# Kernel optimization log

Measured on AMD Instinct MI355X. Metric: run time of the kernel, lower is better.

## Reference

```python
import jax, jax.numpy as jnp
import numpy as np

B, S, D_IN, D_OUT = 4, 2048, 4096, 4096
ACT_CLIP = 6.0

def setup_inputs() -> dict:
    key = jax.random.key(0)
    k1, k2, k3, k4 = jax.random.split(key, 4)
    x = jax.random.normal(k1, (B, S, D_IN), dtype=jnp.float32)
    # symmetric int8 weights in [-127, 127] (stored as int8)
    weight_i8 = jax.random.randint(k2, (D_OUT, D_IN), -127, 128, dtype=jnp.int32).astype(jnp.int8)
    # per-output-channel positive scales, ~ max|w|/127 magnitude
    weight_scale = (jax.random.uniform(k3, (D_OUT,), dtype=jnp.float32) * 0.02 + 1e-4)
    bias = jax.random.normal(k4, (D_OUT,), dtype=jnp.float32)
    return {"x": x, "weight_i8": weight_i8, "weight_scale": weight_scale, "bias": bias}

def reference(x, weight_i8, weight_scale, bias):
    # activation clip
    x = jnp.clip(x, -ACT_CLIP, ACT_CLIP)
    # per-channel dequant: weight[o, i] = i8[o, i] * scale[o]
    weight = weight_i8.astype(jnp.float32) * weight_scale[:, None]
    weight = weight.astype(x.dtype)
    # F.linear: x @ weight.T + bias
    out = jnp.einsum('bsi,oi->bso', x, weight) + bias.astype(x.dtype)
    return out
```

## Files before the change

### kernel.cpp

```cpp
#include <hip/hip_runtime.h>
#include <stdint.h>
#include <stddef.h>


#define M_DIM 8192
#define N_DIM 4096
#define K_DIM 4096
#define ACT_CLIP 6.0f

#define BM 256
#define BN 256
#define BKI 64
#define NKT (K_DIM / BKI)
#define TILE_LDS 32768
#define RING 4

typedef __attribute__((ext_vector_type(4))) int i32x4;
typedef __attribute__((ext_vector_type(16))) int i32x16;

__device__ __forceinline__ void async_load16(const void* g, void* l) {
    __builtin_amdgcn_global_load_lds(
        (const __attribute__((address_space(1))) void*)g,
        (__attribute__((address_space(3))) void*)l, 16, 0, 0);
}

__global__ __launch_bounds__(256) void quant_x_kernel(
    const float* __restrict__ x, int8_t* __restrict__ xq,
    float* __restrict__ rowscale) {
    const int row = blockIdx.x;
    const int tid = threadIdx.x;
    const float4* xr = (const float4*)(x + (size_t)row * K_DIM);
    float4 v[4];
    float mx = 0.f;
#pragma unroll
    for (int c = 0; c < 4; ++c) {
        float4 a = xr[c * 256 + tid];
        a.x = fminf(ACT_CLIP, fmaxf(-ACT_CLIP, a.x));
        a.y = fminf(ACT_CLIP, fmaxf(-ACT_CLIP, a.y));
        a.z = fminf(ACT_CLIP, fmaxf(-ACT_CLIP, a.z));
        a.w = fminf(ACT_CLIP, fmaxf(-ACT_CLIP, a.w));
        v[c] = a;
        mx = fmaxf(mx, fmaxf(fmaxf(fabsf(a.x), fabsf(a.y)),
                             fmaxf(fabsf(a.z), fabsf(a.w))));
    }
#pragma unroll
    for (int off = 32; off >= 1; off >>= 1)
        mx = fmaxf(mx, __shfl_xor(mx, off, 64));
    __shared__ float wmax[4];
    if ((tid & 63) == 0) wmax[tid >> 6] = mx;
    __syncthreads();
    mx = fmaxf(fmaxf(wmax[0], wmax[1]), fmaxf(wmax[2], wmax[3]));
    mx = fmaxf(mx, 1e-20f);
    const float inv = 127.f / mx;
    if (tid == 0) rowscale[row] = mx * (1.f / 127.f);
    int* out = (int*)(xq + (size_t)row * K_DIM);
#pragma unroll
    for (int c = 0; c < 4; ++c) {
        int b0 = (int)rintf(v[c].x * inv);
        int b1 = (int)rintf(v[c].y * inv);
        int b2 = (int)rintf(v[c].z * inv);
        int b3 = (int)rintf(v[c].w * inv);
        out[c * 256 + tid] =
            (b0 & 255) | ((b1 & 255) << 8) | ((b2 & 255) << 16) | ((b3 & 255) << 24);
    }
}

__global__ __launch_bounds__(256) void pack_w_kernel(
    const int* __restrict__ w, int8_t* __restrict__ wq) {
    size_t idx = (size_t)blockIdx.x * blockDim.x + threadIdx.x;
    const int4* w4 = (const int4*)w;
    int r[4];
#pragma unroll
    for (int j = 0; j < 4; ++j) {
        int4 a = w4[idx * 4 + j];
        r[j] = (a.x & 255) | ((a.y & 255) << 8) | ((a.z & 255) << 16) | ((a.w & 255) << 24);
    }
    ((int4*)wq)[idx] = make_int4(r[0], r[1], r[2], r[3]);
}

__global__ __launch_bounds__(512, 2) void gemm_i8_kernel(
    const int8_t* __restrict__ A, const int8_t* __restrict__ Bw,
    const float* __restrict__ rowscale, const float* __restrict__ scale,
    const float* __restrict__ bias, float* __restrict__ out) {
    extern __shared__ __align__(16) int8_t smem[];

    const int tid = threadIdx.x;
    const int wave = tid >> 6;
    const int lane = tid & 63;
    const int l31 = lane & 31;
    const int hi = lane >> 5;
    const int m0 = blockIdx.y * BM;
    const int n0 = blockIdx.x * BN;
    const int wm = (wave >> 2) * 128;
    const int wn = (wave & 3) * 64;

    const int8_t* ga[2];
    const int8_t* gb[2];
    int lbA[2], lbB[2];
#pragma unroll
    for (int j = 0; j < 2; ++j) {
        const int s = tid + 512 * j;
        const int row = s >> 2;
        const int c = (s & 3) ^ ((row >> 1) & 3);
        ga[j] = A + (size_t)(m0 + row) * K_DIM + c * 16;
        gb[j] = Bw + (size_t)(n0 + row) * K_DIM + c * 16;
        lbA[j] = (wave * 64 + 512 * j) * 16;
        lbB[j] = 16384 + (wave * 64 + 512 * j) * 16;
    }

    auto STAGE = [&](int b) {
        int8_t* buf = smem + b * TILE_LDS;
#pragma unroll
        for (int j = 0; j < 2; ++j) async_load16(ga[j], buf + lbA[j]);
#pragma unroll
        for (int j = 0; j < 2; ++j) async_load16(gb[j], buf + lbB[j]);
#pragma unroll
        for (int j = 0; j < 2; ++j) { ga[j] += BKI; gb[j] += BKI; }
    };

    int aoff[4][2], boff[2][2];
#pragma unroll
    for (int mt = 0; mt < 4; ++mt)
#pragma unroll
        for (int ks = 0; ks < 2; ++ks) {
            const int row = wm + mt * 32 + l31;
            const int c = ks * 2 + hi;
            aoff[mt][ks] = (row * 4 + (c ^ ((row >> 1) & 3))) * 16;
        }
#pragma unroll
    for (int nt = 0; nt < 2; ++nt)
#pragma unroll
        for (int ks = 0; ks < 2; ++ks) {
            const int row = wn + nt * 32 + l31;
            const int c = ks * 2 + hi;
            boff[nt][ks] = 16384 + (row * 4 + (c ^ ((row >> 1) & 3))) * 16;
        }

    i32x16 acc[4][2] = {};

    STAGE(0);
    STAGE(1);

    for (int t = 0; t < NKT; ++t) {
        if (t + 2 < NKT) STAGE((t + 2) & 3);
        if (t < NKT - 2) {
            asm volatile("s_waitcnt vmcnt(8)" ::: "memory");
        } else if (t == NKT - 2) {
            asm volatile("s_waitcnt vmcnt(4)" ::: "memory");
        } else {
            asm volatile("s_waitcnt vmcnt(0)" ::: "memory");
        }
        asm volatile("s_barrier" ::: "memory");

        const int8_t* buf = smem + (t & 3) * TILE_LDS;
#pragma unroll
        for (int ks = 0; ks < 2; ++ks) {
            i32x4 af[4], bf[2];
#pragma unroll
            for (int mt = 0; mt < 4; ++mt)
                af[mt] = *(const i32x4*)(buf + aoff[mt][ks]);
#pragma unroll
            for (int nt = 0; nt < 2; ++nt)
                bf[nt] = *(const i32x4*)(buf + boff[nt][ks]);
            __builtin_amdgcn_s_setprio(1);
#pragma unroll
            for (int mt = 0; mt < 4; ++mt)
#pragma unroll
                for (int nt = 0; nt < 2; ++nt)
                    acc[mt][nt] = __builtin_amdgcn_mfma_i32_32x32x32_i8(
                        af[mt], bf[nt], acc[mt][nt], 0, 0, 0);
            __builtin_amdgcn_s_setprio(0);
        }
    }

    const int ccol = l31;
#pragma unroll
    for (int mt = 0; mt < 4; ++mt) {
        const int gmb = m0 + wm + mt * 32;
        float rs[16];
#pragma unroll
        for (int r = 0; r < 16; ++r)
            rs[r] = rowscale[gmb + (r & 3) + 4 * hi + 8 * (r >> 2)];
#pragma unroll
        for (int nt = 0; nt < 2; ++nt) {
            const int gn = n0 + wn + nt * 32 + ccol;
            const float sc = scale[gn];
            const float bi = bias[gn];
            float* op = out + (size_t)gmb * N_DIM + gn;
#pragma unroll
            for (int r = 0; r < 16; ++r) {
                const int grow = (r & 3) + 4 * hi + 8 * (r >> 2);
                op[(size_t)grow * N_DIM] =
                    fmaf((float)acc[mt][nt][r], rs[r] * sc, bi);
            }
        }
    }
}

extern "C" void kernel_launch(void* const* d_in, const int* in_sizes, int n_in,
                              void* d_out, int out_size, void* d_ws, size_t ws_size,
                              hipStream_t stream) {
    const float* x = (const float*)d_in[0];
    const int* w_i8 = (const int*)d_in[1];
    const float* w_scale = (const float*)d_in[2];
    const float* bias = (const float*)d_in[3];
    float* out = (float*)d_out;

    int8_t* xq = (int8_t*)d_ws;
    int8_t* wq = (int8_t*)d_ws + (size_t)M_DIM * K_DIM;
    float* rowscale = (float*)((int8_t*)d_ws + (size_t)M_DIM * K_DIM
                               + (size_t)N_DIM * K_DIM);

    static bool attr_done = false;
    if (!attr_done) {
        hipFuncSetAttribute((const void*)gemm_i8_kernel,
                            hipFuncAttributeMaxDynamicSharedMemorySize,
                            RING * TILE_LDS);
        attr_done = true;
    }

    quant_x_kernel<<<M_DIM, 256, 0, stream>>>(x, xq, rowscale);
    pack_w_kernel<<<(size_t)N_DIM * K_DIM / (16 * 256), 256, 0, stream>>>(w_i8, wq);

    dim3 grid(N_DIM / BN, M_DIM / BM);
    gemm_i8_kernel<<<grid, 512, RING * TILE_LDS, stream>>>(
        xq, wq, rowscale, w_scale, bias, out);
}
```

Baseline: 404.3 us.

## Software-pipeline LDS reads with MFMA in int8 GEMM and merge prep kernels

Restructures the GEMM main loop so LDS fragment reads for the next k-substep are issued before the MFMAs of the current one, with a three-stage prefetch depth and one barrier per tile. It also merges the activation-quantize and weight-pack kernels into a single launch with a branch on block index. The goals are to hide LDS latency behind matrix math and to remove one kernel launch and its tail. It costs more fragment registers under the 2-waves-per-SIMD launch bound, which risks spills.

```diff
diff --git a/kernel.cpp b/kernel.cpp
--- a/kernel.cpp
+++ b/kernel.cpp
@@ -24,58 +24,59 @@
         (__attribute__((address_space(3))) void*)l, 16, 0, 0);
 }
 
-__global__ __launch_bounds__(256) void quant_x_kernel(
+__global__ __launch_bounds__(256) void prep_kernel(
     const float* __restrict__ x, int8_t* __restrict__ xq,
-    float* __restrict__ rowscale) {
-    const int row = blockIdx.x;
+    float* __restrict__ rowscale,
+    const int* __restrict__ w, int8_t* __restrict__ wq) {
     const int tid = threadIdx.x;
-    const float4* xr = (const float4*)(x + (size_t)row * K_DIM);
-    float4 v[4];
-    float mx = 0.f;
-#pragma unroll
-    for (int c = 0; c < 4; ++c) {
-        float4 a = xr[c * 256 + tid];
-        a.x = fminf(ACT_CLIP, fmaxf(-ACT_CLIP, a.x));
-        a.y = fminf(ACT_CLIP, fmaxf(-ACT_CLIP, a.y));
-        a.z = fminf(ACT_CLIP, fmaxf(-ACT_CLIP, a.z));
-        a.w = fminf(ACT_CLIP, fmaxf(-ACT_CLIP, a.w));
-        v[c] = a;
-        mx = fmaxf(mx, fmaxf(fmaxf(fabsf(a.x), fabsf(a.y)),
-                             fmaxf(fabsf(a.z), fabsf(a.w))));
-    }
-#pragma unroll
-    for (int off = 32; off >= 1; off >>= 1)
-        mx = fmaxf(mx, __shfl_xor(mx, off, 64));
-    __shared__ float wmax[4];
-    if ((tid & 63) == 0) wmax[tid >> 6] = mx;
-    __syncthreads();
-    mx = fmaxf(fmaxf(wmax[0], wmax[1]), fmaxf(wmax[2], wmax[3]));
-    mx = fmaxf(mx, 1e-20f);
-    const float inv = 127.f / mx;
-    if (tid == 0) rowscale[row] = mx * (1.f / 127.f);
-    int* out = (int*)(xq + (size_t)row * K_DIM);
-#pragma unroll
-    for (int c = 0; c < 4; ++c) {
-        int b0 = (int)rintf(v[c].x * inv);
-        int b1 = (int)rintf(v[c].y * inv);
-        int b2 = (int)rintf(v[c].z * inv);
-        int b3 = (int)rintf(v[c].w * inv);
-        out[c * 256 + tid] =
-            (b0 & 255) | ((b1 & 255) << 8) | ((b2 & 255) << 16) | ((b3 & 255) << 24);
-    }
-}
-
-__global__ __launch_bounds__(256) void pack_w_kernel(
-    const int* __restrict__ w, int8_t* __restrict__ wq) {
-    size_t idx = (size_t)blockIdx.x * blockDim.x + threadIdx.x;
-    const int4* w4 = (const int4*)w;
-    int r[4];
-#pragma unroll
-    for (int j = 0; j < 4; ++j) {
-        int4 a = w4[idx * 4 + j];
-        r[j] = (a.x & 255) | ((a.y & 255) << 8) | ((a.z & 255) << 16) | ((a.w & 255) << 24);
-    }
-    ((int4*)wq)[idx] = make_int4(r[0], r[1], r[2], r[3]);
+    if (blockIdx.x < M_DIM) {
+        const int row = blockIdx.x;
+        const float4* xr = (const float4*)(x + (size_t)row * K_DIM);
+        float4 v[4];
+        float mx = 0.f;
+#pragma unroll
+        for (int c = 0; c < 4; ++c) {
+            float4 a = xr[c * 256 + tid];
+            a.x = fminf(ACT_CLIP, fmaxf(-ACT_CLIP, a.x));
+            a.y = fminf(ACT_CLIP, fmaxf(-ACT_CLIP, a.y));
+            a.z = fminf(ACT_CLIP, fmaxf(-ACT_CLIP, a.z));
+            a.w = fminf(ACT_CLIP, fmaxf(-ACT_CLIP, a.w));
+            v[c] = a;
+            mx = fmaxf(mx, fmaxf(fmaxf(fabsf(a.x), fabsf(a.y)),
+                                 fmaxf(fabsf(a.z), fabsf(a.w))));
+        }
+#pragma unroll
+        for (int off = 32; off >= 1; off >>= 1)
+            mx = fmaxf(mx, __shfl_xor(mx, off, 64));
+        __shared__ float wmax[4];
+        if ((tid & 63) == 0) wmax[tid >> 6] = mx;
+        __syncthreads();
+        mx = fmaxf(fmaxf(wmax[0], wmax[1]), fmaxf(wmax[2], wmax[3]));
+        mx = fmaxf(mx, 1e-20f);
+        const float inv = 127.f / mx;
+        if (tid == 0) rowscale[row] = mx * (1.f / 127.f);
+        int* out = (int*)(xq + (size_t)row * K_DIM);
+#pragma unroll
+        for (int c = 0; c < 4; ++c) {
+            int b0 = (int)rintf(v[c].x * inv);
+            int b1 = (int)rintf(v[c].y * inv);
+            int b2 = (int)rintf(v[c].z * inv);
+            int b3 = (int)rintf(v[c].w * inv);
+            out[c * 256 + tid] =
+                (b0 & 255) | ((b1 & 255) << 8) | ((b2 & 255) << 16) | ((b3 & 255) << 24);
+        }
+    } else {
+        size_t idx = (size_t)(blockIdx.x - M_DIM) * 256 + tid;
+        const int4* w4 = (const int4*)w;
+        int r[4];
+#pragma unroll
+        for (int j = 0; j < 4; ++j) {
+            int4 a = w4[idx * 4 + j];
+            r[j] = (a.x & 255) | ((a.y & 255) << 8) | ((a.z & 255) << 16) |
+                   ((a.w & 255) << 24);
+        }
+        ((int4*)wq)[idx] = make_int4(r[0], r[1], r[2], r[3]);
+    }
 }
 
 __global__ __launch_bounds__(512, 2) void gemm_i8_kernel(
@@ -118,60 +119,78 @@
         for (int j = 0; j < 2; ++j) { ga[j] += BKI; gb[j] += BKI; }
     };
 
-    int aoff[4][2], boff[2][2];
-#pragma unroll
-    for (int mt = 0; mt < 4; ++mt)
-#pragma unroll
-        for (int ks = 0; ks < 2; ++ks) {
-            const int row = wm + mt * 32 + l31;
-            const int c = ks * 2 + hi;
-            aoff[mt][ks] = (row * 4 + (c ^ ((row >> 1) & 3))) * 16;
-        }
-#pragma unroll
-    for (int nt = 0; nt < 2; ++nt)
-#pragma unroll
-        for (int ks = 0; ks < 2; ++ks) {
-            const int row = wn + nt * 32 + l31;
-            const int c = ks * 2 + hi;
-            boff[nt][ks] = 16384 + (row * 4 + (c ^ ((row >> 1) & 3))) * 16;
-        }
-
+    const int swz = (l31 >> 1) & 3;
+    const int abase0 = (wm + l31) * 64 + ((0 * 2 + hi) ^ swz) * 16;
+    const int abase1 = (wm + l31) * 64 + ((1 * 2 + hi) ^ swz) * 16;
+    const int bbase0 = 16384 + (wn + l31) * 64 + ((0 * 2 + hi) ^ swz) * 16;
+    const int bbase1 = 16384 + (wn + l31) * 64 + ((1 * 2 + hi) ^ swz) * 16;
+
+    i32x4 a0[4], b0[2], a1[4], b1[2];
     i32x16 acc[4][2] = {};
+
+    auto READ0 = [&](const int8_t* buf) {
+#pragma unroll
+        for (int mt = 0; mt < 4; ++mt)
+            a0[mt] = *(const i32x4*)(buf + abase0 + mt * 2048);
+#pragma unroll
+        for (int nt = 0; nt < 2; ++nt)
+            b0[nt] = *(const i32x4*)(buf + bbase0 + nt * 2048);
+    };
+    auto READ1 = [&](const int8_t* buf) {
+#pragma unroll
+        for (int mt = 0; mt < 4; ++mt)
+            a1[mt] = *(const i32x4*)(buf + abase1 + mt * 2048);
+#pragma unroll
+        for (int nt = 0; nt < 2; ++nt)
+            b1[nt] = *(const i32x4*)(buf + bbase1 + nt * 2048);
+    };
+    auto MFMA0 = [&]() {
+        __builtin_amdgcn_s_setprio(1);
+#pragma unroll
+        for (int mt = 0; mt < 4; ++mt)
+#pragma unroll
+            for (int nt = 0; nt < 2; ++nt)
+                acc[mt][nt] = __builtin_amdgcn_mfma_i32_32x32x32_i8(
+                    a0[mt], b0[nt], acc[mt][nt], 0, 0, 0);
+        __builtin_amdgcn_s_setprio(0);
+    };
+    auto MFMA1 = [&]() {
+        __builtin_amdgcn_s_setprio(1);
+#pragma unroll
+        for (int mt = 0; mt < 4; ++mt)
+#pragma unroll
+            for (int nt = 0; nt < 2; ++nt)
+                acc[mt][nt] = __builtin_amdgcn_mfma_i32_32x32x32_i8(
+                    a1[mt], b1[nt], acc[mt][nt], 0, 0, 0);
+        __builtin_amdgcn_s_setprio(0);
+    };
 
     STAGE(0);
     STAGE(1);
-
-    for (int t = 0; t < NKT; ++t) {
-        if (t + 2 < NKT) STAGE((t + 2) & 3);
-        if (t < NKT - 2) {
+    STAGE(2);
+    asm volatile("s_waitcnt vmcnt(8)" ::: "memory");
+    asm volatile("s_barrier" ::: "memory");
+    READ0(smem);
+
+    for (int t = 0; t < NKT - 1; ++t) {
+        if (t + 3 < NKT) STAGE((t + 3) & 3);
+        READ1(smem + (t & 3) * TILE_LDS);
+        MFMA0();
+        if (t < NKT - 3) {
             asm volatile("s_waitcnt vmcnt(8)" ::: "memory");
-        } else if (t == NKT - 2) {
+        } else if (t == NKT - 3) {
             asm volatile("s_waitcnt vmcnt(4)" ::: "memory");
         } else {
             asm volatile("s_waitcnt vmcnt(0)" ::: "memory");
         }
         asm volatile("s_barrier" ::: "memory");
-
-        const int8_t* buf = smem + (t & 3) * TILE_LDS;
-#pragma unroll
-        for (int ks = 0; ks < 2; ++ks) {
-            i32x4 af[4], bf[2];
-#pragma unroll
-            for (int mt = 0; mt < 4; ++mt)
-                af[mt] = *(const i32x4*)(buf + aoff[mt][ks]);
-#pragma unroll
-            for (int nt = 0; nt < 2; ++nt)
-                bf[nt] = *(const i32x4*)(buf + boff[nt][ks]);
-            __builtin_amdgcn_s_setprio(1);
-#pragma unroll
-            for (int mt = 0; mt < 4; ++mt)
-#pragma unroll
-                for (int nt = 0; nt < 2; ++nt)
-                    acc[mt][nt] = __builtin_amdgcn_mfma_i32_32x32x32_i8(
-                        af[mt], bf[nt], acc[mt][nt], 0, 0, 0);
-            __builtin_amdgcn_s_setprio(0);
-        }
-    }
+        __builtin_amdgcn_sched_barrier(0);
+        READ0(smem + ((t + 1) & 3) * TILE_LDS);
+        MFMA1();
+    }
+    READ1(smem + ((NKT - 1) & 3) * TILE_LDS);
+    MFMA0();
+    MFMA1();
 
     const int ccol = l31;
 #pragma unroll
@@ -219,8 +238,8 @@
         attr_done = true;
     }
 
-    quant_x_kernel<<<M_DIM, 256, 0, stream>>>(x, xq, rowscale);
-    pack_w_kernel<<<(size_t)N_DIM * K_DIM / (16 * 256), 256, 0, stream>>>(w_i8, wq);
+    const int pack_blocks = (int)((size_t)N_DIM * K_DIM / (16 * 256));
+    prep_kernel<<<M_DIM + pack_blocks, 256, 0, stream>>>(x, xq, rowscale, w_i8, wq);
 
     dim3 grid(N_DIM / BN, M_DIM / BM);
     gemm_i8_kernel<<<grid, 512, RING * TILE_LDS, stream>>>(
```

Result: faster. 395.0 us (-2.3%).

## Shrink GEMM tile to 256x128 with 256 threads, 3-stage ring, fuse prep kernels

Applied to the files above, without the earlier changes.

Changes the int8 GEMM block tile from 256x256 with 8 waves to 256x128 with 4 waves. Each wave still computes a 128x64 output. The LDS ring drops from 4 to 3 stages, and the wait and barrier move after the MFMAs, with all fragments loaded up front. The activation quantisation and weight packing kernels are merged into one launch to save launch overhead. The smaller tile lowers LDS use so more blocks can be resident, at the cost of less B reuse and more A global traffic per output.

```diff
diff --git a/kernel.cpp b/kernel.cpp
--- a/kernel.cpp
+++ b/kernel.cpp
@@ -9,11 +9,13 @@
 #define ACT_CLIP 6.0f
 
 #define BM 256
-#define BN 256
+#define BN 128
 #define BKI 64
 #define NKT (K_DIM / BKI)
-#define TILE_LDS 32768
-#define RING 4
+#define A_BYTES (BM * BKI)
+#define B_BYTES (BN * BKI)
+#define TILE_LDS (A_BYTES + B_BYTES)
+#define RING 3
 
 typedef __attribute__((ext_vector_type(4))) int i32x4;
 typedef __attribute__((ext_vector_type(16))) int i32x16;
@@ -24,61 +26,62 @@
         (__attribute__((address_space(3))) void*)l, 16, 0, 0);
 }
 
-__global__ __launch_bounds__(256) void quant_x_kernel(
+__global__ __launch_bounds__(256) void prep_kernel(
     const float* __restrict__ x, int8_t* __restrict__ xq,
-    float* __restrict__ rowscale) {
-    const int row = blockIdx.x;
+    float* __restrict__ rowscale,
+    const int* __restrict__ w, int8_t* __restrict__ wq) {
     const int tid = threadIdx.x;
-    const float4* xr = (const float4*)(x + (size_t)row * K_DIM);
-    float4 v[4];
-    float mx = 0.f;
-#pragma unroll
-    for (int c = 0; c < 4; ++c) {
-        float4 a = xr[c * 256 + tid];
-        a.x = fminf(ACT_CLIP, fmaxf(-ACT_CLIP, a.x));
-        a.y = fminf(ACT_CLIP, fmaxf(-ACT_CLIP, a.y));
-        a.z = fminf(ACT_CLIP, fmaxf(-ACT_CLIP, a.z));
-        a.w = fminf(ACT_CLIP, fmaxf(-ACT_CLIP, a.w));
-        v[c] = a;
-        mx = fmaxf(mx, fmaxf(fmaxf(fabsf(a.x), fabsf(a.y)),
-                             fmaxf(fabsf(a.z), fabsf(a.w))));
-    }
-#pragma unroll
-    for (int off = 32; off >= 1; off >>= 1)
-        mx = fmaxf(mx, __shfl_xor(mx, off, 64));
-    __shared__ float wmax[4];
-    if ((tid & 63) == 0) wmax[tid >> 6] = mx;
-    __syncthreads();
-    mx = fmaxf(fmaxf(wmax[0], wmax[1]), fmaxf(wmax[2], wmax[3]));
-    mx = fmaxf(mx, 1e-20f);
-    const float inv = 127.f / mx;
-    if (tid == 0) rowscale[row] = mx * (1.f / 127.f);
-    int* out = (int*)(xq + (size_t)row * K_DIM);
-#pragma unroll
-    for (int c = 0; c < 4; ++c) {
-        int b0 = (int)rintf(v[c].x * inv);
-        int b1 = (int)rintf(v[c].y * inv);
-        int b2 = (int)rintf(v[c].z * inv);
-        int b3 = (int)rintf(v[c].w * inv);
-        out[c * 256 + tid] =
-            (b0 & 255) | ((b1 & 255) << 8) | ((b2 & 255) << 16) | ((b3 & 255) << 24);
-    }
-}
-
-__global__ __launch_bounds__(256) void pack_w_kernel(
-    const int* __restrict__ w, int8_t* __restrict__ wq) {
-    size_t idx = (size_t)blockIdx.x * blockDim.x + threadIdx.x;
-    const int4* w4 = (const int4*)w;
-    int r[4];
-#pragma unroll
-    for (int j = 0; j < 4; ++j) {
-        int4 a = w4[idx * 4 + j];
-        r[j] = (a.x & 255) | ((a.y & 255) << 8) | ((a.z & 255) << 16) | ((a.w & 255) << 24);
-    }
-    ((int4*)wq)[idx] = make_int4(r[0], r[1], r[2], r[3]);
-}
-
-__global__ __launch_bounds__(512, 2) void gemm_i8_kernel(
+    if (blockIdx.x < M_DIM) {
+        const int row = blockIdx.x;
+        const float4* xr = (const float4*)(x + (size_t)row * K_DIM);
+        float4 v[4];
+        float mx = 0.f;
+#pragma unroll
+        for (int c = 0; c < 4; ++c) {
+            float4 a = xr[c * 256 + tid];
+            a.x = fminf(ACT_CLIP, fmaxf(-ACT_CLIP, a.x));
+            a.y = fminf(ACT_CLIP, fmaxf(-ACT_CLIP, a.y));
+            a.z = fminf(ACT_CLIP, fmaxf(-ACT_CLIP, a.z));
+            a.w = fminf(ACT_CLIP, fmaxf(-ACT_CLIP, a.w));
+            v[c] = a;
+            mx = fmaxf(mx, fmaxf(fmaxf(fabsf(a.x), fabsf(a.y)),
+                                 fmaxf(fabsf(a.z), fabsf(a.w))));
+        }
+#pragma unroll
+        for (int off = 32; off >= 1; off >>= 1)
+            mx = fmaxf(mx, __shfl_xor(mx, off, 64));
+        __shared__ float wmax[4];
+        if ((tid & 63) == 0) wmax[tid >> 6] = mx;
+        __syncthreads();
+        mx = fmaxf(fmaxf(wmax[0], wmax[1]), fmaxf(wmax[2], wmax[3]));
+        mx = fmaxf(mx, 1e-20f);
+        const float inv = 127.f / mx;
+        if (tid == 0) rowscale[row] = mx * (1.f / 127.f);
+        int* out = (int*)(xq + (size_t)row * K_DIM);
+#pragma unroll
+        for (int c = 0; c < 4; ++c) {
+            int b0 = (int)rintf(v[c].x * inv);
+            int b1 = (int)rintf(v[c].y * inv);
+            int b2 = (int)rintf(v[c].z * inv);
+            int b3 = (int)rintf(v[c].w * inv);
+            out[c * 256 + tid] =
+                (b0 & 255) | ((b1 & 255) << 8) | ((b2 & 255) << 16) | ((b3 & 255) << 24);
+        }
+    } else {
+        size_t idx = (size_t)(blockIdx.x - M_DIM) * 256 + tid;
+        const int4* w4 = (const int4*)w;
+        int r[4];
+#pragma unroll
+        for (int j = 0; j < 4; ++j) {
+            int4 a = w4[idx * 4 + j];
+            r[j] = (a.x & 255) | ((a.y & 255) << 8) | ((a.z & 255) << 16) |
+                   ((a.w & 255) << 24);
+        }
+        ((int4*)wq)[idx] = make_int4(r[0], r[1], r[2], r[3]);
+    }
+}
+
+__global__ __launch_bounds__(256, 2) void gemm_i8_kernel(
     const int8_t* __restrict__ A, const int8_t* __restrict__ Bw,
     const float* __restrict__ rowscale, const float* __restrict__ scale,
     const float* __restrict__ bias, float* __restrict__ out) {
@@ -91,86 +94,88 @@
     const int hi = lane >> 5;
     const int m0 = blockIdx.y * BM;
     const int n0 = blockIdx.x * BN;
-    const int wm = (wave >> 2) * 128;
-    const int wn = (wave & 3) * 64;
-
-    const int8_t* ga[2];
+    const int wm = (wave >> 1) * 128;
+    const int wn = (wave & 1) * 64;
+
+    const int8_t* ga[4];
     const int8_t* gb[2];
-    int lbA[2], lbB[2];
-#pragma unroll
-    for (int j = 0; j < 2; ++j) {
-        const int s = tid + 512 * j;
+    int lbA[4], lbB[2];
+#pragma unroll
+    for (int j = 0; j < 4; ++j) {
+        const int s = tid + 256 * j;
         const int row = s >> 2;
         const int c = (s & 3) ^ ((row >> 1) & 3);
         ga[j] = A + (size_t)(m0 + row) * K_DIM + c * 16;
+        lbA[j] = (wave * 64 + 256 * j) * 16;
+    }
+#pragma unroll
+    for (int j = 0; j < 2; ++j) {
+        const int s = tid + 256 * j;
+        const int row = s >> 2;
+        const int c = (s & 3) ^ ((row >> 1) & 3);
         gb[j] = Bw + (size_t)(n0 + row) * K_DIM + c * 16;
-        lbA[j] = (wave * 64 + 512 * j) * 16;
-        lbB[j] = 16384 + (wave * 64 + 512 * j) * 16;
+        lbB[j] = A_BYTES + (wave * 64 + 256 * j) * 16;
     }
 
     auto STAGE = [&](int b) {
         int8_t* buf = smem + b * TILE_LDS;
 #pragma unroll
-        for (int j = 0; j < 2; ++j) async_load16(ga[j], buf + lbA[j]);
+        for (int j = 0; j < 4; ++j) async_load16(ga[j], buf + lbA[j]);
 #pragma unroll
         for (int j = 0; j < 2; ++j) async_load16(gb[j], buf + lbB[j]);
 #pragma unroll
-        for (int j = 0; j < 2; ++j) { ga[j] += BKI; gb[j] += BKI; }
+        for (int j = 0; j < 4; ++j) ga[j] += BKI;
+#pragma unroll
+        for (int j = 0; j < 2; ++j) gb[j] += BKI;
     };
 
-    int aoff[4][2], boff[2][2];
-#pragma unroll
-    for (int mt = 0; mt < 4; ++mt)
-#pragma unroll
-        for (int ks = 0; ks < 2; ++ks) {
-            const int row = wm + mt * 32 + l31;
-            const int c = ks * 2 + hi;
-            aoff[mt][ks] = (row * 4 + (c ^ ((row >> 1) & 3))) * 16;
-        }
-#pragma unroll
-    for (int nt = 0; nt < 2; ++nt)
-#pragma unroll
-        for (int ks = 0; ks < 2; ++ks) {
-            const int row = wn + nt * 32 + l31;
-            const int c = ks * 2 + hi;
-            boff[nt][ks] = 16384 + (row * 4 + (c ^ ((row >> 1) & 3))) * 16;
-        }
+    const int swz = (l31 >> 1) & 3;
+    const int abase = (wm + l31) * 64;
+    const int bbase = A_BYTES + (wn + l31) * 64;
+    int koff[2];
+#pragma unroll
+    for (int ks = 0; ks < 2; ++ks) koff[ks] = ((ks * 2 + hi) ^ swz) * 16;
 
     i32x16 acc[4][2] = {};
 
     STAGE(0);
     STAGE(1);
-
+    asm volatile("s_waitcnt vmcnt(6)" ::: "memory");
+    asm volatile("s_barrier" ::: "memory");
+
+    int cur = 0, stg = 2;
     for (int t = 0; t < NKT; ++t) {
-        if (t + 2 < NKT) STAGE((t + 2) & 3);
-        if (t < NKT - 2) {
-            asm volatile("s_waitcnt vmcnt(8)" ::: "memory");
-        } else if (t == NKT - 2) {
-            asm volatile("s_waitcnt vmcnt(4)" ::: "memory");
-        } else {
-            asm volatile("s_waitcnt vmcnt(0)" ::: "memory");
-        }
-        asm volatile("s_barrier" ::: "memory");
-
-        const int8_t* buf = smem + (t & 3) * TILE_LDS;
+        if (t + 2 < NKT) STAGE(stg);
+
+        const int8_t* buf = smem + cur * TILE_LDS;
+        i32x4 af[4][2], bf[2][2];
 #pragma unroll
         for (int ks = 0; ks < 2; ++ks) {
-            i32x4 af[4], bf[2];
 #pragma unroll
             for (int mt = 0; mt < 4; ++mt)
-                af[mt] = *(const i32x4*)(buf + aoff[mt][ks]);
+                af[mt][ks] = *(const i32x4*)(buf + abase + mt * 2048 + koff[ks]);
 #pragma unroll
             for (int nt = 0; nt < 2; ++nt)
-                bf[nt] = *(const i32x4*)(buf + boff[nt][ks]);
-            __builtin_amdgcn_s_setprio(1);
+                bf[nt][ks] = *(const i32x4*)(buf + bbase + nt * 2048 + koff[ks]);
+        }
+#pragma unroll
+        for (int ks = 0; ks < 2; ++ks)
 #pragma unroll
             for (int mt = 0; mt < 4; ++mt)
 #pragma unroll
                 for (int nt = 0; nt < 2; ++nt)
                     acc[mt][nt] = __builtin_amdgcn_mfma_i32_32x32x32_i8(
-                        af[mt], bf[nt], acc[mt][nt], 0, 0, 0);
-            __builtin_amdgcn_s_setprio(0);
-        }
+                        af[mt][ks], bf[nt][ks], acc[mt][nt], 0, 0, 0);
+
+        if (t < NKT - 2) {
+            asm volatile("s_waitcnt vmcnt(6)" ::: "memory");
+            asm volatile("s_barrier" ::: "memory");
+        } else if (t == NKT - 2) {
+            asm volatile("s_waitcnt vmcnt(0)" ::: "memory");
+            asm volatile("s_barrier" ::: "memory");
+        }
+        cur = (cur == 2) ? 0 : cur + 1;
+        stg = (stg == 2) ? 0 : stg + 1;
     }
 
     const int ccol = l31;
@@ -219,10 +224,10 @@
         attr_done = true;
     }
 
-    quant_x_kernel<<<M_DIM, 256, 0, stream>>>(x, xq, rowscale);
-    pack_w_kernel<<<(size_t)N_DIM * K_DIM / (16 * 256), 256, 0, stream>>>(w_i8, wq);
+    const int pack_blocks = (int)((size_t)N_DIM * K_DIM / (16 * 256));
+    prep_kernel<<<M_DIM + pack_blocks, 256, 0, stream>>>(x, xq, rowscale, w_i8, wq);
 
     dim3 grid(N_DIM / BN, M_DIM / BM);
-    gemm_i8_kernel<<<grid, 512, RING * TILE_LDS, stream>>>(
+    gemm_i8_kernel<<<grid, 256, RING * TILE_LDS, stream>>>(
         xq, wq, rowscale, w_scale, bias, out);
 }
```

New measurement: 413.1 us. +2.2%, slower.

## Double-buffer 128-wide K tiles with interleaved async loads and merge prep kernels

Applied to the files above, without the earlier changes.

Replaces the 4-deep ring of 64-byte K tiles with two 64KB buffers holding 128-byte K tiles, issuing the next tile's async global-to-LDS loads spread across the first sub-steps of the current tile's MFMA loop, with an 8-way XOR swizzle. It also fuses the activation-quantize and weight-pack kernels into one launch. The aim is fewer outer iterations and waits per K and one less kernel launch, at the cost of shallower prefetch distance and more barriers per tile.

```diff
diff --git a/kernel.cpp b/kernel.cpp
--- a/kernel.cpp
+++ b/kernel.cpp
@@ -10,10 +10,10 @@
 
 #define BM 256
 #define BN 256
-#define BKI 64
-#define NKT (K_DIM / BKI)
-#define TILE_LDS 32768
-#define RING 4
+#define BKB 128
+#define NKT (K_DIM / BKB)
+#define B_OFF 32768
+#define BUF_BYTES 65536
 
 typedef __attribute__((ext_vector_type(4))) int i32x4;
 typedef __attribute__((ext_vector_type(16))) int i32x16;
@@ -24,58 +24,59 @@
         (__attribute__((address_space(3))) void*)l, 16, 0, 0);
 }
 
-__global__ __launch_bounds__(256) void quant_x_kernel(
+__global__ __launch_bounds__(256) void prep_kernel(
     const float* __restrict__ x, int8_t* __restrict__ xq,
-    float* __restrict__ rowscale) {
-    const int row = blockIdx.x;
+    float* __restrict__ rowscale,
+    const int* __restrict__ w, int8_t* __restrict__ wq) {
     const int tid = threadIdx.x;
-    const float4* xr = (const float4*)(x + (size_t)row * K_DIM);
-    float4 v[4];
-    float mx = 0.f;
-#pragma unroll
-    for (int c = 0; c < 4; ++c) {
-        float4 a = xr[c * 256 + tid];
-        a.x = fminf(ACT_CLIP, fmaxf(-ACT_CLIP, a.x));
-        a.y = fminf(ACT_CLIP, fmaxf(-ACT_CLIP, a.y));
-        a.z = fminf(ACT_CLIP, fmaxf(-ACT_CLIP, a.z));
-        a.w = fminf(ACT_CLIP, fmaxf(-ACT_CLIP, a.w));
-        v[c] = a;
-        mx = fmaxf(mx, fmaxf(fmaxf(fabsf(a.x), fabsf(a.y)),
-                             fmaxf(fabsf(a.z), fabsf(a.w))));
-    }
-#pragma unroll
-    for (int off = 32; off >= 1; off >>= 1)
-        mx = fmaxf(mx, __shfl_xor(mx, off, 64));
-    __shared__ float wmax[4];
-    if ((tid & 63) == 0) wmax[tid >> 6] = mx;
-    __syncthreads();
-    mx = fmaxf(fmaxf(wmax[0], wmax[1]), fmaxf(wmax[2], wmax[3]));
-    mx = fmaxf(mx, 1e-20f);
-    const float inv = 127.f / mx;
-    if (tid == 0) rowscale[row] = mx * (1.f / 127.f);
-    int* out = (int*)(xq + (size_t)row * K_DIM);
-#pragma unroll
-    for (int c = 0; c < 4; ++c) {
-        int b0 = (int)rintf(v[c].x * inv);
-        int b1 = (int)rintf(v[c].y * inv);
-        int b2 = (int)rintf(v[c].z * inv);
-        int b3 = (int)rintf(v[c].w * inv);
-        out[c * 256 + tid] =
-            (b0 & 255) | ((b1 & 255) << 8) | ((b2 & 255) << 16) | ((b3 & 255) << 24);
-    }
-}
-
-__global__ __launch_bounds__(256) void pack_w_kernel(
-    const int* __restrict__ w, int8_t* __restrict__ wq) {
-    size_t idx = (size_t)blockIdx.x * blockDim.x + threadIdx.x;
-    const int4* w4 = (const int4*)w;
-    int r[4];
-#pragma unroll
-    for (int j = 0; j < 4; ++j) {
-        int4 a = w4[idx * 4 + j];
-        r[j] = (a.x & 255) | ((a.y & 255) << 8) | ((a.z & 255) << 16) | ((a.w & 255) << 24);
-    }
-    ((int4*)wq)[idx] = make_int4(r[0], r[1], r[2], r[3]);
+    if (blockIdx.x < M_DIM) {
+        const int row = blockIdx.x;
+        const float4* xr = (const float4*)(x + (size_t)row * K_DIM);
+        float4 v[4];
+        float mx = 0.f;
+#pragma unroll
+        for (int c = 0; c < 4; ++c) {
+            float4 a = xr[c * 256 + tid];
+            a.x = fminf(ACT_CLIP, fmaxf(-ACT_CLIP, a.x));
+            a.y = fminf(ACT_CLIP, fmaxf(-ACT_CLIP, a.y));
+            a.z = fminf(ACT_CLIP, fmaxf(-ACT_CLIP, a.z));
+            a.w = fminf(ACT_CLIP, fmaxf(-ACT_CLIP, a.w));
+            v[c] = a;
+            mx = fmaxf(mx, fmaxf(fmaxf(fabsf(a.x), fabsf(a.y)),
+                                 fmaxf(fabsf(a.z), fabsf(a.w))));
+        }
+#pragma unroll
+        for (int off = 32; off >= 1; off >>= 1)
+            mx = fmaxf(mx, __shfl_xor(mx, off, 64));
+        __shared__ float wmax[4];
+        if ((tid & 63) == 0) wmax[tid >> 6] = mx;
+        __syncthreads();
+        mx = fmaxf(fmaxf(wmax[0], wmax[1]), fmaxf(wmax[2], wmax[3]));
+        mx = fmaxf(mx, 1e-20f);
+        const float inv = 127.f / mx;
+        if (tid == 0) rowscale[row] = mx * (1.f / 127.f);
+        int* out = (int*)(xq + (size_t)row * K_DIM);
+#pragma unroll
+        for (int c = 0; c < 4; ++c) {
+            int b0 = (int)rintf(v[c].x * inv);
+            int b1 = (int)rintf(v[c].y * inv);
+            int b2 = (int)rintf(v[c].z * inv);
+            int b3 = (int)rintf(v[c].w * inv);
+            out[c * 256 + tid] =
+                (b0 & 255) | ((b1 & 255) << 8) | ((b2 & 255) << 16) | ((b3 & 255) << 24);
+        }
+    } else {
+        size_t idx = (size_t)(blockIdx.x - M_DIM) * 256 + tid;
+        const int4* w4 = (const int4*)w;
+        int r[4];
+#pragma unroll
+        for (int j = 0; j < 4; ++j) {
+            int4 a = w4[idx * 4 + j];
+            r[j] = (a.x & 255) | ((a.y & 255) << 8) | ((a.z & 255) << 16) |
+                   ((a.w & 255) << 24);
+        }
+        ((int4*)wq)[idx] = make_int4(r[0], r[1], r[2], r[3]);
+    }
 }
 
 __global__ __launch_bounds__(512, 2) void gemm_i8_kernel(
@@ -94,74 +95,64 @@
     const int wm = (wave >> 2) * 128;
     const int wn = (wave & 3) * 64;
 
-    const int8_t* ga[2];
-    const int8_t* gb[2];
-    int lbA[2], lbB[2];
-#pragma unroll
-    for (int j = 0; j < 2; ++j) {
-        const int s = tid + 512 * j;
-        const int row = s >> 2;
-        const int c = (s & 3) ^ ((row >> 1) & 3);
-        ga[j] = A + (size_t)(m0 + row) * K_DIM + c * 16;
-        gb[j] = Bw + (size_t)(n0 + row) * K_DIM + c * 16;
-        lbA[j] = (wave * 64 + 512 * j) * 16;
-        lbB[j] = 16384 + (wave * 64 + 512 * j) * 16;
-    }
-
-    auto STAGE = [&](int b) {
-        int8_t* buf = smem + b * TILE_LDS;
-#pragma unroll
-        for (int j = 0; j < 2; ++j) async_load16(ga[j], buf + lbA[j]);
-#pragma unroll
-        for (int j = 0; j < 2; ++j) async_load16(gb[j], buf + lbB[j]);
-#pragma unroll
-        for (int j = 0; j < 2; ++j) { ga[j] += BKI; gb[j] += BKI; }
-    };
-
-    int aoff[4][2], boff[2][2];
-#pragma unroll
-    for (int mt = 0; mt < 4; ++mt)
-#pragma unroll
-        for (int ks = 0; ks < 2; ++ks) {
-            const int row = wm + mt * 32 + l31;
-            const int c = ks * 2 + hi;
-            aoff[mt][ks] = (row * 4 + (c ^ ((row >> 1) & 3))) * 16;
-        }
-#pragma unroll
-    for (int nt = 0; nt < 2; ++nt)
-#pragma unroll
-        for (int ks = 0; ks < 2; ++ks) {
-            const int row = wn + nt * 32 + l31;
-            const int c = ks * 2 + hi;
-            boff[nt][ks] = 16384 + (row * 4 + (c ^ ((row >> 1) & 3))) * 16;
-        }
+    const int8_t* gsA[4];
+    const int8_t* gsB[4];
+    int ldA[4], ldB[4];
+#pragma unroll
+    for (int i = 0; i < 4; ++i) {
+        const int s = i * 512 + tid;
+        const int row = s >> 3;
+        const int c = (s & 7) ^ (row & 7);
+        gsA[i] = A + (size_t)(m0 + row) * K_DIM + c * 16;
+        gsB[i] = Bw + (size_t)(n0 + row) * K_DIM + c * 16;
+        ldA[i] = (i * 512 + wave * 64) * 16;
+        ldB[i] = B_OFF + (i * 512 + wave * 64) * 16;
+    }
+
+    const int sw = l31 & 7;
+    const int abase = (wm + l31) * BKB;
+    const int bbase = B_OFF + (wn + l31) * BKB;
+    int koff[4];
+#pragma unroll
+    for (int kc = 0; kc < 4; ++kc) koff[kc] = ((kc * 2 + hi) ^ sw) * 16;
 
     i32x16 acc[4][2] = {};
 
-    STAGE(0);
-    STAGE(1);
+#pragma unroll
+    for (int i = 0; i < 4; ++i) {
+        async_load16(gsA[i], smem + ldA[i]);
+        async_load16(gsB[i], smem + ldB[i]);
+        gsA[i] += BKB;
+        gsB[i] += BKB;
+    }
+    asm volatile("s_waitcnt vmcnt(0)" ::: "memory");
+    __builtin_amdgcn_s_barrier();
 
     for (int t = 0; t < NKT; ++t) {
-        if (t + 2 < NKT) STAGE((t + 2) & 3);
-        if (t < NKT - 2) {
-            asm volatile("s_waitcnt vmcnt(8)" ::: "memory");
-        } else if (t == NKT - 2) {
-            asm volatile("s_waitcnt vmcnt(4)" ::: "memory");
-        } else {
-            asm volatile("s_waitcnt vmcnt(0)" ::: "memory");
-        }
-        asm volatile("s_barrier" ::: "memory");
-
-        const int8_t* buf = smem + (t & 3) * TILE_LDS;
-#pragma unroll
-        for (int ks = 0; ks < 2; ++ks) {
+        const int8_t* buf = smem + (size_t)(t & 1) * BUF_BYTES;
+        int8_t* nbuf = smem + (size_t)((t + 1) & 1) * BUF_BYTES;
+        const bool more = (t + 1 < NKT);
+#pragma unroll
+        for (int kc = 0; kc < 4; ++kc) {
             i32x4 af[4], bf[2];
 #pragma unroll
             for (int mt = 0; mt < 4; ++mt)
-                af[mt] = *(const i32x4*)(buf + aoff[mt][ks]);
+                af[mt] = *(const i32x4*)(buf + abase + mt * 4096 + koff[kc]);
 #pragma unroll
             for (int nt = 0; nt < 2; ++nt)
-                bf[nt] = *(const i32x4*)(buf + boff[nt][ks]);
+                bf[nt] = *(const i32x4*)(buf + bbase + nt * 4096 + koff[kc]);
+            if (more && kc < 2) {
+#pragma unroll
+                for (int i = kc * 2; i < kc * 2 + 2; ++i) {
+                    async_load16(gsA[i], nbuf + ldA[i]);
+                    async_load16(gsB[i], nbuf + ldB[i]);
+                    gsA[i] += BKB;
+                    gsB[i] += BKB;
+                }
+            }
+            __builtin_amdgcn_s_barrier();
+            asm volatile("s_waitcnt lgkmcnt(0)" ::: "memory");
+            __builtin_amdgcn_sched_barrier(0);
             __builtin_amdgcn_s_setprio(1);
 #pragma unroll
             for (int mt = 0; mt < 4; ++mt)
@@ -170,6 +161,10 @@
                     acc[mt][nt] = __builtin_amdgcn_mfma_i32_32x32x32_i8(
                         af[mt], bf[nt], acc[mt][nt], 0, 0, 0);
             __builtin_amdgcn_s_setprio(0);
+            if (kc == 3) {
+                asm volatile("s_waitcnt vmcnt(0)" ::: "memory");
+            }
+            __builtin_amdgcn_s_barrier();
         }
     }
 
@@ -215,14 +210,14 @@
     if (!attr_done) {
         hipFuncSetAttribute((const void*)gemm_i8_kernel,
                             hipFuncAttributeMaxDynamicSharedMemorySize,
-                            RING * TILE_LDS);
+                            2 * BUF_BYTES);
         attr_done = true;
     }
 
-    quant_x_kernel<<<M_DIM, 256, 0, stream>>>(x, xq, rowscale);
-    pack_w_kernel<<<(size_t)N_DIM * K_DIM / (16 * 256), 256, 0, stream>>>(w_i8, wq);
+    const int pack_blocks = (int)((size_t)N_DIM * K_DIM / (16 * 256));
+    prep_kernel<<<M_DIM + pack_blocks, 256, 0, stream>>>(x, xq, rowscale, w_i8, wq);
 
     dim3 grid(N_DIM / BN, M_DIM / BM);
-    gemm_i8_kernel<<<grid, 512, RING * TILE_LDS, stream>>>(
+    gemm_i8_kernel<<<grid, 512, 2 * BUF_BYTES, stream>>>(
         xq, wq, rowscale, w_scale, bias, out);
 }
```

After: 400.8 us. No clear change (-0.9%).
